# Optimization experiments

Hardware: AMD Instinct MI355X
Metric: run time of the kernel (lower is better)

The kernel has to match this reference:

```python
import jax, jax.numpy as jnp
import numpy as np

B, T, D, E = 4, 2048, 1024, 8


def setup_inputs() -> dict:
    key = jax.random.key(0)
    ks = jax.random.split(key, 8)
    scale_g = float(np.sqrt(2.0 / (D + E)))  # xavier_uniform-ish scale for W_g
    scale_w = float(1.0 / np.sqrt(D))
    return {
        "x": jax.random.normal(ks[0], (B, T, D), dtype=jnp.float32),
        "noise": jax.random.normal(ks[1], (B, T, E), dtype=jnp.float32),  # the N(0,1) sample in Gating.forward
        "W_g": jax.random.normal(ks[2], (D, E), dtype=jnp.float32) * scale_g,
        "W_noise": jax.random.normal(ks[3], (D, E), dtype=jnp.float32),
        "W1": jax.random.normal(ks[4], (E, D, D), dtype=jnp.float32) * scale_w,
        "b1": jnp.zeros((E, D), dtype=jnp.float32),
        "W2": jax.random.normal(ks[5], (E, D, D), dtype=jnp.float32) * scale_w,
        "b2": jnp.zeros((E, D), dtype=jnp.float32),
        "k": 2,
    }


def _gates(x, noise, W_g, W_noise, k):
    # h = x@W_g + N(0,1) + softplus(x@W_noise)   (note: noise added, not scaled)
    h = jnp.einsum("btd,de->bte", x, W_g) + noise + jax.nn.softplus(
        jnp.einsum("btd,de->bte", x, W_noise)
    )
    kth = jax.lax.top_k(h, k)[0][..., -1:]           # kth largest per token
    h_masked = jnp.where(h >= kth, h, -jnp.inf)       # keepTopK (ties kept, as in torch)
    return jax.nn.softmax(h_masked, axis=-1)          # [B,T,E]


def reference(x, noise, W_g, W_noise, W1, b1, W2, b2, k):
    gates = _gates(x, noise, W_g, W_noise, k)
    # Dense loop over experts (faithful to original): every expert FFN on all tokens.
    # hidden: [E,B,T,D]
    hidden = jax.nn.relu(jnp.einsum("btd,edh->ebth", x, W1) + b1[:, None, None, :])
    expert_out = jnp.einsum("ebth,eho->ebto", hidden, W2) + b2[:, None, None, :]
    # mask-weighted combine: sum_e expert_out_e * gates[...,e]
    return jnp.einsum("ebtd,bte->btd", expert_out, gates)
```

## Files before the change

kernel.cpp:

```cpp
#include <hip/hip_runtime.h>
#include <hip/hip_bf16.h>

#define BTOK 8192
#define DDIM 1024
#define NEXP 8

typedef unsigned short u16;
typedef unsigned int u32;
typedef __attribute__((ext_vector_type(8))) short short8;
typedef __attribute__((ext_vector_type(4))) float f32x4;

constexpr int BM = 256, BN = 256, BK = 64;
constexpr int SLOTCAP = 3072;
constexpr int NT = DDIM / BK;

__device__ __forceinline__ u16 f2bf(float f){
  __hip_bfloat16 h = __float2bfloat16(f);
  return *reinterpret_cast<u16*>(&h);
}
__device__ __forceinline__ float bf2f(u16 v){
  return __uint_as_float(((u32)v) << 16);
}
__device__ __forceinline__ void gll16(const u16* gsrc, u16* ldst){
  __builtin_amdgcn_global_load_lds((const __attribute__((address_space(1))) void*)gsrc,
                                   (__attribute__((address_space(3))) void*)ldst,
                                   16, 0, 0);
}

__global__ __launch_bounds__(256) void wprep_kernel(
    const float* __restrict__ Wg, const float* __restrict__ Wn,
    u16* __restrict__ wpt)
{
  const int idx = blockIdx.x*256 + threadIdx.x;
  const int n = idx >> 10, d = idx & 1023;
  const float v = (n < 8) ? Wg[d*8 + n] : Wn[d*8 + (n-8)];
  const u16 hi = f2bf(v);
  const u16 lo = f2bf(v - bf2f(hi));
  wpt[n*1024 + d]          = hi;
  wpt[16384 + n*1024 + d]  = lo;
}

__global__ __launch_bounds__(128) void score_kernel(
    const float* __restrict__ x, const u16* __restrict__ wpt,
    float* __restrict__ hp, u16* __restrict__ xb)
{
  __shared__ __align__(16) u16 lw[2][16][1024];
  const int tid = threadIdx.x;
  const int wave = tid >> 6, lane = tid & 63;

  for (int it = 0; it < 32; ++it){
    const int cid = it*128 + tid;
    const int v = cid >> 11, rem = cid & 2047;
    const int n = rem >> 7, c = rem & 127;
    const short8 val = *reinterpret_cast<const short8*>(wpt + v*16384 + n*1024 + c*8);
    *reinterpret_cast<short8*>(&lw[v][n][(c ^ (n&7))*8]) = val;
  }
  __syncthreads();

  const int q = lane >> 4, l16 = lane & 15;
  const int t0 = blockIdx.x*32 + wave*16;
  const int rowA = t0 + l16;
  const float* xp  = x  + (size_t)rowA*DDIM + q*8;
  u16*         xbo = xb + (size_t)rowA*DDIM + q*8;

  f32x4 acc0 = {0.f,0.f,0.f,0.f}, acc1 = acc0, acc2 = acc0;
  for (int kt = 0; kt < 32; ++kt){
    const float4 x0 = *reinterpret_cast<const float4*>(xp + kt*32);
    const float4 x1 = *reinterpret_cast<const float4*>(xp + kt*32 + 4);
    short8 ah;
    ah[0]=(short)f2bf(x0.x); ah[1]=(short)f2bf(x0.y);
    ah[2]=(short)f2bf(x0.z); ah[3]=(short)f2bf(x0.w);
    ah[4]=(short)f2bf(x1.x); ah[5]=(short)f2bf(x1.y);
    ah[6]=(short)f2bf(x1.z); ah[7]=(short)f2bf(x1.w);
    *reinterpret_cast<short8*>(xbo + kt*32) = ah;
    short8 al;
    al[0]=(short)f2bf(x0.x - bf2f((u16)ah[0])); al[1]=(short)f2bf(x0.y - bf2f((u16)ah[1]));
    al[2]=(short)f2bf(x0.z - bf2f((u16)ah[2])); al[3]=(short)f2bf(x0.w - bf2f((u16)ah[3]));
    al[4]=(short)f2bf(x1.x - bf2f((u16)ah[4])); al[5]=(short)f2bf(x1.y - bf2f((u16)ah[5]));
    al[6]=(short)f2bf(x1.z - bf2f((u16)ah[6])); al[7]=(short)f2bf(x1.w - bf2f((u16)ah[7]));
    const int bs = ((kt*4 + q) ^ (l16 & 7)) * 8;
    const short8 bh = *reinterpret_cast<const short8*>(&lw[0][l16][bs]);
    const short8 bl = *reinterpret_cast<const short8*>(&lw[1][l16][bs]);
    acc0 = __builtin_amdgcn_mfma_f32_16x16x32_bf16(ah, bh, acc0, 0, 0, 0);
    acc1 = __builtin_amdgcn_mfma_f32_16x16x32_bf16(al, bh, acc1, 0, 0, 0);
    acc2 = __builtin_amdgcn_mfma_f32_16x16x32_bf16(ah, bl, acc2, 0, 0, 0);
  }
  #pragma unroll
  for (int r = 0; r < 4; ++r)
    hp[(size_t)(t0 + q*4 + r)*16 + l16] = acc0[r] + acc1[r] + acc2[r];
}

__global__ __launch_bounds__(256) void gating_select_kernel(
    const float* __restrict__ hp, const float* __restrict__ noise,
    const int* __restrict__ kp,
    float* __restrict__ gates, int* __restrict__ counts, int* __restrict__ lists,
    int* __restrict__ tokmap, int* __restrict__ ncnt)
{
  __shared__ int lcnt[NEXP];
  __shared__ int lbase[NEXP];
  const int tid = threadIdx.x;
  const int t   = blockIdx.x*256 + tid;
  if (tid < NEXP) lcnt[tid] = 0;
  __syncthreads();

  float hg[16];
  #pragma unroll
  for (int i = 0; i < 4; ++i){
    const float4 v = reinterpret_cast<const float4*>(hp + (size_t)t*16)[i];
    hg[i*4+0]=v.x; hg[i*4+1]=v.y; hg[i*4+2]=v.z; hg[i*4+3]=v.w;
  }
  float h[NEXP];
  #pragma unroll
  for (int e = 0; e < NEXP; ++e){
    const float hn = hg[8+e];
    const float sp = (hn > 20.f) ? hn : log1pf(expf(hn));
    h[e] = hg[e] + noise[(size_t)t*NEXP + e] + sp;
  }

  int kk = *kp; kk = kk<1?1:(kk>NEXP?NEXP:kk);
  bool used[NEXP];
  #pragma unroll
  for (int e=0;e<NEXP;e++) used[e]=false;
  float kth = 0.f;
  for (int i=0;i<kk;i++){
    int bi=0; float bv=-3.4e38f;
    #pragma unroll
    for (int e=0;e<NEXP;e++) if (!used[e] && h[e]>bv){bv=h[e]; bi=e;}
    used[bi]=true; kth=bv;
  }
  float m=-3.4e38f;
  #pragma unroll
  for (int e=0;e<NEXP;e++) if (h[e]>=kth && h[e]>m) m=h[e];
  float p[NEXP], s=0.f;
  #pragma unroll
  for (int e=0;e<NEXP;e++){ p[e]=(h[e]>=kth)?expf(h[e]-m):0.f; s+=p[e]; }
  const float inv = 1.f/s;
  float g[NEXP];
  int lslot[NEXP];
  #pragma unroll
  for (int e=0;e<NEXP;e++){
    g[e] = p[e]*inv;
    gates[(size_t)t*NEXP + e] = g[e];
    if (g[e] > 0.f) lslot[e] = atomicAdd(&lcnt[e], 1);
  }
  __syncthreads();
  if (tid < NEXP) lbase[tid] = atomicAdd(&counts[tid], lcnt[tid]);
  __syncthreads();
  int idx = 0;
  #pragma unroll
  for (int e=0;e<NEXP;e++){
    if (g[e] > 0.f){
      const int slot = lbase[e] + lslot[e];
      lists[e*BTOK + slot] = t;
      tokmap[t*NEXP + idx] = (e << 13) | (slot & 8191);
      idx++;
    }
  }
  ncnt[t] = idx;
}

__global__ __launch_bounds__(256) void trans_kernel(
    const float* __restrict__ W1, const float* __restrict__ W2,
    u16* __restrict__ W1T, u16* __restrict__ W2T)
{
  __shared__ float tile[64][65];
  const int mz = blockIdx.z;
  const float* src = (mz < NEXP) ? (W1  + (size_t)mz*DDIM*DDIM) : (W2  + (size_t)(mz-NEXP)*DDIM*DDIM);
  u16*       dst = (mz < NEXP) ? (W1T + (size_t)mz*DDIM*DDIM) : (W2T + (size_t)(mz-NEXP)*DDIM*DDIM);
  const int r0 = blockIdx.x*64, c0 = blockIdx.y*64;
  const int tx = threadIdx.x & 63, ty = threadIdx.x >> 6;
  #pragma unroll
  for (int i=ty;i<64;i+=4)
    tile[i][tx] = src[(size_t)(r0+i)*DDIM + c0+tx];
  __syncthreads();
  #pragma unroll
  for (int i=ty;i<64;i+=4)
    dst[(size_t)(c0+i)*DDIM + r0+tx] = f2bf(tile[tx][i]);
}

template<int LAYER>
__device__ __forceinline__ void ffn_body(
    const u16* __restrict__ Asrc, const u16* __restrict__ WT,
    const float* __restrict__ bias,
    const int* __restrict__ counts, const int* __restrict__ lists,
    u16* __restrict__ dst)
{
  const int lin = blockIdx.x;
  const int e   = lin & 7;
  const int idx = lin >> 3;
  const int m0  = (idx >> 2) * BM;
  const int n0  = (idx & 3)  * BN;
  int cnt = counts[e]; if (cnt > SLOTCAP) cnt = SLOTCAP;
  if (m0 >= cnt) return;

  __shared__ __align__(16) u16 ldsA[2][BM*BK];
  __shared__ __align__(16) u16 ldsB[2][BN*BK];

  const int tid = threadIdx.x;
  const int wave = tid>>6, lane = tid&63;
  const int wm = wave>>2, wn = wave&3;

  const u16* aSrc[4]; const u16* bSrc[4];
  {
    const int lr = lane>>3, sp = lane&7;
    #pragma unroll
    for (int i=0;i<4;i++){
      const int row = wave*32 + i*8 + lr;
      const int ku  = sp ^ (row&7);
      size_t abase;
      if constexpr (LAYER==1){
        int gr = m0 + row; if (gr >= cnt) gr = cnt-1;
        abase = (size_t)lists[e*BTOK + gr] * DDIM;
      } else {
        abase = ((size_t)e*SLOTCAP + m0 + row) * DDIM;
      }
      aSrc[i] = Asrc + abase + ku*8;
      bSrc[i] = WT + ((size_t)e*DDIM + n0 + row)*DDIM + ku*8;
    }
  }

  const int q = lane>>4, l16 = lane&15;
  int aoff[8], boff[4];
  #pragma unroll
  for (int f=0;f<8;f++){
    const int ra = wm*128 + f*16 + l16;
    aoff[f] = ra*BK + ((q ^ (ra&7))*8);
  }
  #pragma unroll
  for (int f=0;f<4;f++){
    const int rb = wn*64 + f*16 + l16;
    boff[f] = rb*BK + ((q ^ (rb&7))*8);
  }

  f32x4 acc[8][4];
  #pragma unroll
  for (int i=0;i<8;i++)
    #pragma unroll
    for (int j=0;j<4;j++)
      acc[i][j] = (f32x4){0.f,0.f,0.f,0.f};

  #define STAGE(T, c)                                            \
    _Pragma("unroll")                                            \
    for (int i=0;i<4;i++){                                       \
      gll16(aSrc[i] + (size_t)(T)*BK, &ldsA[c][(wave*32+i*8)*BK]); \
      gll16(bSrc[i] + (size_t)(T)*BK, &ldsB[c][(wave*32+i*8)*BK]); \
    }

  STAGE(0, 0)
  __syncthreads();
  int cur = 0;
  for (int kt = 0; kt < NT; ++kt){
    if (kt + 1 < NT) STAGE(kt+1, cur^1)
    #pragma unroll
    for (int kk=0; kk<2; kk++){
      const int kx = kk ? 32 : 0;
      short8 bfr[4], afr[8];
      #pragma unroll
      for (int f=0;f<4;f++) bfr[f] = *reinterpret_cast<const short8*>(&ldsB[cur][boff[f] ^ kx]);
      #pragma unroll
      for (int f=0;f<8;f++) afr[f] = *reinterpret_cast<const short8*>(&ldsA[cur][aoff[f] ^ kx]);
      __builtin_amdgcn_s_setprio(1);
      #pragma unroll
      for (int fm=0;fm<8;fm++)
        #pragma unroll
        for (int fn=0;fn<4;fn++)
          acc[fm][fn] = __builtin_amdgcn_mfma_f32_16x16x32_bf16(afr[fm], bfr[fn], acc[fm][fn], 0, 0, 0);
      __builtin_amdgcn_s_setprio(0);
    }
    __syncthreads();
    cur ^= 1;
  }
  #undef STAGE

  #pragma unroll
  for (int fm=0;fm<8;fm++){
    #pragma unroll
    for (int r=0;r<4;r++){
      const int row = wm*128 + fm*16 + q*4 + r;
      const int gr  = m0 + row;
      #pragma unroll
      for (int fn=0;fn<4;fn++){
        const int col = n0 + wn*64 + fn*16 + l16;
        float v = acc[fm][fn][r] + bias[e*DDIM + col];
        if constexpr (LAYER==1) v = v > 0.f ? v : 0.f;
        dst[((size_t)e*SLOTCAP + gr)*DDIM + col] = f2bf(v);
      }
    }
  }
}

__global__ __launch_bounds__(512, 1) void ffn1_kernel(
    const u16* __restrict__ A, const u16* __restrict__ WT, const float* __restrict__ b,
    const int* __restrict__ counts, const int* __restrict__ lists, u16* __restrict__ dst)
{ ffn_body<1>(A, WT, b, counts, lists, dst); }

__global__ __launch_bounds__(512, 1) void ffn2_kernel(
    const u16* __restrict__ A, const u16* __restrict__ WT, const float* __restrict__ b,
    const int* __restrict__ counts, const int* __restrict__ lists, u16* __restrict__ dst)
{ ffn_body<2>(A, WT, b, counts, lists, dst); }

__global__ __launch_bounds__(256) void combine_kernel(
    const u16* __restrict__ partial, const int* __restrict__ tokmap,
    const int* __restrict__ ncnt, const float* __restrict__ gates,
    float* __restrict__ out)
{
  const int t = blockIdx.x, c = threadIdx.x;
  const int n = ncnt[t];
  float4 acc = {0.f, 0.f, 0.f, 0.f};
  for (int j = 0; j < n; ++j){
    const int ent  = tokmap[t*NEXP + j];
    const int e    = ent >> 13, slot = ent & 8191;
    if (slot >= SLOTCAP) continue;
    const float g = gates[(size_t)t*NEXP + e];
    const ushort4 pv = reinterpret_cast<const ushort4*>(
        partial + ((size_t)e*SLOTCAP + slot)*DDIM)[c];
    acc.x = fmaf(g, bf2f(pv.x), acc.x);
    acc.y = fmaf(g, bf2f(pv.y), acc.y);
    acc.z = fmaf(g, bf2f(pv.z), acc.z);
    acc.w = fmaf(g, bf2f(pv.w), acc.w);
  }
  reinterpret_cast<float4*>(out + (size_t)t*DDIM)[c] = acc;
}

extern "C" void kernel_launch(void* const* d_in, const int* in_sizes, int n_in,
                              void* d_out, int out_size, void* d_ws, size_t ws_size,
                              hipStream_t stream)
{
  const float* x     = (const float*)d_in[0];
  const float* noise = (const float*)d_in[1];
  const float* Wg    = (const float*)d_in[2];
  const float* Wn    = (const float*)d_in[3];
  const float* W1    = (const float*)d_in[4];
  const float* b1    = (const float*)d_in[5];
  const float* W2    = (const float*)d_in[6];
  const float* b2    = (const float*)d_in[7];
  const int*   kp    = (const int*)d_in[8];
  float* out = (float*)d_out;

  char* ws = (char*)d_ws;
  int*   counts = (int*)ws;
  int*   lists  = (int*)(ws + 4096);
  float* gates  = (float*)(ws + 266240);
  int*   tokmap = (int*)(ws + 528384);
  int*   ncnt   = (int*)(ws + 790528);
  u16*   xb     = (u16*)(ws + 823296);
  u16*   W1T    = (u16*)(ws + 17600512);
  u16*   W2T    = (u16*)(ws + 34377728);
  u16*   hidden = (u16*)(ws + 51154944);
  u16*   partial= (u16*)(ws + 101486592);
  float* hp     = (float*)(ws + 101486592);
  u16*   wpt    = (u16*)(ws + 102010880);
  const size_t NEED = 151818240ull;

  hipMemsetAsync(counts, 0, 64, stream);
  if (ws_size < NEED){
    hipMemsetAsync(d_out, 0, (size_t)out_size*sizeof(float), stream);
    return;
  }

  wprep_kernel<<<64, 256, 0, stream>>>(Wg, Wn, wpt);
  trans_kernel<<<dim3(16,16,16), 256, 0, stream>>>(W1, W2, W1T, W2T);
  score_kernel<<<BTOK/32, 128, 0, stream>>>(x, wpt, hp, xb);
  gating_select_kernel<<<BTOK/256, 256, 0, stream>>>(hp, noise, kp, gates, counts, lists,
                                                     tokmap, ncnt);
  ffn1_kernel<<<(SLOTCAP/BM)*4*NEXP, 512, 0, stream>>>(
      xb, W1T, b1, counts, lists, hidden);
  ffn2_kernel<<<(SLOTCAP/BM)*4*NEXP, 512, 0, stream>>>(
      hidden, W2T, b2, counts, lists, partial);
  combine_kernel<<<BTOK, 256, 0, stream>>>(partial, tokmap, ncnt, gates, out);
}
```

Before: 324.0 us.

## Split expert GEMM tails into separate small-tile ragged kernels

The big 256x256 FFN kernels now process only full 256-row tiles per expert. A new ragged kernel with 64-row tiles handles the remaining partial rows after each FFN layer. This avoids computing padded rows of the last partial 256-row tile. The cost is two extra kernel launches, and the tail work runs on only a few small blocks serialized after the main GEMM.

```diff
diff --git a/kernel.cpp b/kernel.cpp
--- a/kernel.cpp
+++ b/kernel.cpp
@@ -13,6 +13,7 @@
 constexpr int BM = 256, BN = 256, BK = 64;
 constexpr int SLOTCAP = 3072;
 constexpr int NT = DDIM / BK;
+constexpr int RBM = 64, RBN = 256;
 
 __device__ __forceinline__ u16 f2bf(float f){
   __hip_bfloat16 h = __float2bfloat16(f);
@@ -191,7 +192,7 @@
   const int m0  = (idx >> 2) * BM;
   const int n0  = (idx & 3)  * BN;
   int cnt = counts[e]; if (cnt > SLOTCAP) cnt = SLOTCAP;
-  if (m0 >= cnt) return;
+  if (m0 + BM > cnt) return;
 
   __shared__ __align__(16) u16 ldsA[2][BM*BK];
   __shared__ __align__(16) u16 ldsB[2][BN*BK];
@@ -209,8 +210,7 @@
       const int ku  = sp ^ (row&7);
       size_t abase;
       if constexpr (LAYER==1){
-        int gr = m0 + row; if (gr >= cnt) gr = cnt-1;
-        abase = (size_t)lists[e*BTOK + gr] * DDIM;
+        abase = (size_t)lists[e*BTOK + m0 + row] * DDIM;
       } else {
         abase = ((size_t)e*SLOTCAP + m0 + row) * DDIM;
       }
@@ -298,6 +298,127 @@
     const u16* __restrict__ A, const u16* __restrict__ WT, const float* __restrict__ b,
     const int* __restrict__ counts, const int* __restrict__ lists, u16* __restrict__ dst)
 { ffn_body<2>(A, WT, b, counts, lists, dst); }
+
+template<int LAYER>
+__device__ __forceinline__ void ragged_body(
+    const u16* __restrict__ Asrc, const u16* __restrict__ WT,
+    const float* __restrict__ bias,
+    const int* __restrict__ counts, const int* __restrict__ lists,
+    u16* __restrict__ dst)
+{
+  const int lin = blockIdx.x;
+  const int e   = lin & 7;
+  const int r2  = lin >> 3;
+  const int rs  = r2 >> 2;
+  const int nt  = r2 & 3;
+  int cnt = counts[e]; if (cnt > SLOTCAP) cnt = SLOTCAP;
+  const int base = (cnt >> 8) << 8;
+  const int m0 = base + rs*RBM;
+  if (m0 >= cnt) return;
+  const int n0 = nt * RBN;
+
+  __shared__ __align__(16) u16 ldsA[2][RBM*BK];
+  __shared__ __align__(16) u16 ldsB[2][RBN*BK];
+
+  const int tid = threadIdx.x;
+  const int wave = tid>>6, lane = tid&63;
+  const int lr = lane>>3, sp = lane&7;
+
+  const u16* aSrc[2]; const u16* bSrc[8];
+  #pragma unroll
+  for (int i=0;i<2;i++){
+    const int row = wave*16 + i*8 + lr;
+    const int ku  = sp ^ (row&7);
+    int gr = m0 + row; if (gr >= cnt) gr = cnt-1;
+    size_t abase;
+    if constexpr (LAYER==1) abase = (size_t)lists[e*BTOK + gr] * DDIM;
+    else                    abase = ((size_t)e*SLOTCAP + gr) * DDIM;
+    aSrc[i] = Asrc + abase + ku*8;
+  }
+  #pragma unroll
+  for (int i=0;i<8;i++){
+    const int row = wave*64 + i*8 + lr;
+    const int ku  = sp ^ (row&7);
+    bSrc[i] = WT + ((size_t)e*DDIM + n0 + row)*DDIM + ku*8;
+  }
+
+  const int q = lane>>4, l16 = lane&15;
+  int aoff[4], boff[4];
+  #pragma unroll
+  for (int f=0;f<4;f++){
+    const int ra = f*16 + l16;
+    aoff[f] = ra*BK + ((q ^ (ra&7))*8);
+    const int rb = wave*64 + f*16 + l16;
+    boff[f] = rb*BK + ((q ^ (rb&7))*8);
+  }
+
+  f32x4 acc[4][4];
+  #pragma unroll
+  for (int i=0;i<4;i++)
+    #pragma unroll
+    for (int j=0;j<4;j++)
+      acc[i][j] = (f32x4){0.f,0.f,0.f,0.f};
+
+  #define RSTAGE(T, c)                                             \
+    _Pragma("unroll")                                              \
+    for (int i=0;i<2;i++)                                          \
+      gll16(aSrc[i] + (size_t)(T)*BK, &ldsA[c][(wave*16+i*8)*BK]); \
+    _Pragma("unroll")                                              \
+    for (int i=0;i<8;i++)                                          \
+      gll16(bSrc[i] + (size_t)(T)*BK, &ldsB[c][(wave*64+i*8)*BK]);
+
+  RSTAGE(0, 0)
+  __syncthreads();
+  int cur = 0;
+  for (int kt = 0; kt < NT; ++kt){
+    if (kt + 1 < NT) { RSTAGE(kt+1, cur^1) }
+    #pragma unroll
+    for (int kk=0; kk<2; kk++){
+      const int kx = kk ? 32 : 0;
+      short8 afr[4], bfr[4];
+      #pragma unroll
+      for (int f=0;f<4;f++) afr[f] = *reinterpret_cast<const short8*>(&ldsA[cur][aoff[f] ^ kx]);
+      #pragma unroll
+      for (int f=0;f<4;f++) bfr[f] = *reinterpret_cast<const short8*>(&ldsB[cur][boff[f] ^ kx]);
+      #pragma unroll
+      for (int fm=0;fm<4;fm++)
+        #pragma unroll
+        for (int fn=0;fn<4;fn++)
+          acc[fm][fn] = __builtin_amdgcn_mfma_f32_16x16x32_bf16(afr[fm], bfr[fn], acc[fm][fn], 0, 0, 0);
+    }
+    __syncthreads();
+    cur ^= 1;
+  }
+  #undef RSTAGE
+
+  #pragma unroll
+  for (int fm=0;fm<4;fm++){
+    #pragma unroll
+    for (int r=0;r<4;r++){
+      const int row = fm*16 + q*4 + r;
+      const int gr  = m0 + row;
+      if (gr < cnt){
+        #pragma unroll
+        for (int fn=0;fn<4;fn++){
+          const int col = n0 + wave*64 + fn*16 + l16;
+          float v = acc[fm][fn][r] + bias[e*DDIM + col];
+          if constexpr (LAYER==1) v = v > 0.f ? v : 0.f;
+          dst[((size_t)e*SLOTCAP + gr)*DDIM + col] = f2bf(v);
+        }
+      }
+    }
+  }
+}
+
+__global__ __launch_bounds__(256, 1) void ragged1_kernel(
+    const u16* __restrict__ A, const u16* __restrict__ WT, const float* __restrict__ b,
+    const int* __restrict__ counts, const int* __restrict__ lists, u16* __restrict__ dst)
+{ ragged_body<1>(A, WT, b, counts, lists, dst); }
+
+__global__ __launch_bounds__(256, 1) void ragged2_kernel(
+    const u16* __restrict__ A, const u16* __restrict__ WT, const float* __restrict__ b,
+    const int* __restrict__ counts, const int* __restrict__ lists, u16* __restrict__ dst)
+{ ragged_body<2>(A, WT, b, counts, lists, dst); }
 
 __global__ __launch_bounds__(256) void combine_kernel(
     const u16* __restrict__ partial, const int* __restrict__ tokmap,
@@ -365,7 +486,11 @@
                                                      tokmap, ncnt);
   ffn1_kernel<<<(SLOTCAP/BM)*4*NEXP, 512, 0, stream>>>(
       xb, W1T, b1, counts, lists, hidden);
+  ragged1_kernel<<<128, 256, 0, stream>>>(
+      xb, W1T, b1, counts, lists, hidden);
   ffn2_kernel<<<(SLOTCAP/BM)*4*NEXP, 512, 0, stream>>>(
       hidden, W2T, b2, counts, lists, partial);
+  ragged2_kernel<<<128, 256, 0, stream>>>(
+      hidden, W2T, b2, counts, lists, partial);
   combine_kernel<<<BTOK, 256, 0, stream>>>(partial, tokmap, ncnt, gates, out);
 }
```

Result: no change. 319.4 us (-1.4%).
